# Optimization experiments

Hardware: AMD Instinct MI355X
Metric: run time of the kernel (lower is better)

The kernel has to match this reference:

```python
import jax, jax.numpy as jnp
import numpy as np


def setup_inputs() -> dict:
    key = jax.random.key(0)
    k1, k2 = jax.random.split(key)
    D, N, M = 256, 1024, 1024
    z_x = jax.random.normal(k1, (1, D, N), dtype=jnp.float32)
    z_y = jax.random.normal(k2, (1, D, M), dtype=jnp.float32)
    return {"z_x": z_x, "z_y": z_y}


def reference(z_x, z_y):
    # squeeze().t(): (1, d, N) -> (N, d)
    x = jnp.squeeze(z_x).T  # (N, d)
    y = jnp.squeeze(z_y).T  # (M, d)
    # L1 compare: s[i, j] = -sum_d |x[i, d] - y[j, d]|  -> (N, M)
    s = -jnp.sum(jnp.abs(x[:, None, :] - y[None, :, :]), axis=-1)
    a = jax.nn.softmax(s, axis=1)  # row-wise softmax
    b = jax.nn.softmax(s, axis=0)  # column-wise softmax
    a = a + b - a * b              # soft union of alignments
    return jnp.sum(a * s) / jnp.sum(a)
```

## Files before the change

### kernel.cpp

```cpp
#include <hip/hip_runtime.h>
#include <math.h>


#define DD 256
#define NN 1024
#define DS 4
#define CH (DD / DS)

__device__ __forceinline__ float waveMax(float v) {
  #pragma unroll
  for (int off = 32; off; off >>= 1) v = fmaxf(v, __shfl_xor(v, off, 64));
  return v;
}
__device__ __forceinline__ float waveSum(float v) {
  #pragma unroll
  for (int off = 32; off; off >>= 1) v += __shfl_xor(v, off, 64);
  return v;
}
__device__ __forceinline__ float blockMax(float v, float* red) {
  v = waveMax(v);
  __syncthreads();
  if ((threadIdx.x & 63) == 0) red[threadIdx.x >> 6] = v;
  __syncthreads();
  return fmaxf(fmaxf(red[0], red[1]), fmaxf(red[2], red[3]));
}
__device__ __forceinline__ float blockSum(float v, float* red) {
  v = waveSum(v);
  __syncthreads();
  if ((threadIdx.x & 63) == 0) red[threadIdx.x >> 6] = v;
  __syncthreads();
  return red[0] + red[1] + red[2] + red[3];
}


__global__ __launch_bounds__(256)
void scompute_kernel(const float* __restrict__ zx, const float* __restrict__ zy,
                     float* __restrict__ Sp, float* __restrict__ accum) {
  const int h  = blockIdx.z;
  const int i0 = blockIdx.y * 64;
  const int j0 = blockIdx.x * 128;
  const int t  = threadIdx.x;
  const int g  = t >> 5;
  const int c  = t & 31;
  if ((blockIdx.x | blockIdx.y | blockIdx.z) == 0 && t == 0) {
    accum[0] = 0.f; accum[1] = 0.f;
  }

  __shared__ float xs[CH * 64];
  {
    const float4* __restrict__ X4 = (const float4*)zx;
    float4* xs4 = (float4*)xs;
    #pragma unroll
    for (int k = t; k < CH * 16; k += 256)
      xs4[k] = X4[(h * CH + (k >> 4)) * (NN / 4) + (i0 >> 2) + (k & 15)];
  }
  __syncthreads();

  float acc[8][4];
  #pragma unroll
  for (int r = 0; r < 8; ++r)
    #pragma unroll
    for (int q = 0; q < 4; ++q) acc[r][q] = 0.f;

  const float4* __restrict__ yp =
      (const float4*)zy + (size_t)(h * CH) * (NN / 4) + (j0 >> 2) + c;
  #pragma unroll 4
  for (int d = 0; d < CH; ++d) {
    const float4 yv = yp[d * (NN / 4)];
    const float* xr = xs + d * 64 + g * 8;
    #pragma unroll
    for (int r = 0; r < 8; ++r) {
      const float xv = xr[r];
      acc[r][0] += fabsf(xv - yv.x);
      acc[r][1] += fabsf(xv - yv.y);
      acc[r][2] += fabsf(xv - yv.z);
      acc[r][3] += fabsf(xv - yv.w);
    }
  }

  float4* __restrict__ S4 = (float4*)Sp + (size_t)h * (NN * NN / 4);
  #pragma unroll
  for (int r = 0; r < 8; ++r)
    S4[(i0 + g * 8 + r) * (NN / 4) + (j0 >> 2) + c] =
        make_float4(acc[r][0], acc[r][1], acc[r][2], acc[r][3]);
}

__global__ __launch_bounds__(256)
void rowstats_kernel(float* __restrict__ Sp,
                     float* __restrict__ rmax, float* __restrict__ rsum) {
  __shared__ float red[4];
  const int t = threadIdx.x;
  const int row0 = blockIdx.x * 4;
  float4* S4 = (float4*)Sp;
  #pragma unroll
  for (int rr = 0; rr < 4; ++rr) {
    const int row = row0 + rr;
    float4 p = S4[row * (NN / 4) + t];
    #pragma unroll
    for (int hh = 1; hh < DS; ++hh) {
      const float4 q = S4[hh * (NN * NN / 4) + row * (NN / 4) + t];
      p.x += q.x; p.y += q.y; p.z += q.z; p.w += q.w;
    }
    S4[row * (NN / 4) + t] = p;
    float m = fmaxf(fmaxf(-p.x, -p.y), fmaxf(-p.z, -p.w));
    m = blockMax(m, red);
    float l = __expf(-p.x - m) + __expf(-p.y - m) +
              __expf(-p.z - m) + __expf(-p.w - m);
    l = blockSum(l, red);
    if (t == 0) { rmax[row] = m; rsum[row] = l; }
  }
}

__global__ __launch_bounds__(256)
void colstats_kernel(const float* __restrict__ Sp,
                     float* __restrict__ pm, float* __restrict__ ps) {
  const int t = threadIdx.x;
  const int r0 = blockIdx.x * 16;
  const float4* S4 = (const float4*)Sp;
  float4 m = make_float4(-1e30f, -1e30f, -1e30f, -1e30f);
  #pragma unroll 4
  for (int i = 0; i < 16; ++i) {
    const float4 p = S4[(r0 + i) * (NN / 4) + t];
    m.x = fmaxf(m.x, -p.x); m.y = fmaxf(m.y, -p.y);
    m.z = fmaxf(m.z, -p.z); m.w = fmaxf(m.w, -p.w);
  }
  float4 l = make_float4(0.f, 0.f, 0.f, 0.f);
  #pragma unroll 4
  for (int i = 0; i < 16; ++i) {
    const float4 p = S4[(r0 + i) * (NN / 4) + t];
    l.x += __expf(-p.x - m.x); l.y += __expf(-p.y - m.y);
    l.z += __expf(-p.z - m.z); l.w += __expf(-p.w - m.w);
  }
  ((float4*)pm)[blockIdx.x * (NN / 4) + t] = m;
  ((float4*)ps)[blockIdx.x * (NN / 4) + t] = l;
}

__global__ __launch_bounds__(256)
void colcombine_kernel(const float* __restrict__ pm, const float* __restrict__ ps,
                       float* __restrict__ cmax, float* __restrict__ csum) {
  const int j = blockIdx.x * 256 + threadIdx.x;
  float m = -1e30f;
  #pragma unroll 8
  for (int k = 0; k < 64; ++k) m = fmaxf(m, pm[k * NN + j]);
  float l = 0.f;
  #pragma unroll 8
  for (int k = 0; k < 64; ++k) l += __expf(pm[k * NN + j] - m) * ps[k * NN + j];
  cmax[j] = m; csum[j] = l;
}

__global__ __launch_bounds__(256)
void final_kernel(const float* __restrict__ Sp,
                  const float* __restrict__ rmax, const float* __restrict__ rsum,
                  const float* __restrict__ cmax, const float* __restrict__ csum,
                  float* __restrict__ accum) {
  __shared__ float redn[4], redd[4];
  const int t = threadIdx.x;
  const int row0 = blockIdx.x * 4;
  const float4* S4 = (const float4*)Sp;
  const float4 cm = ((const float4*)cmax)[t];
  const float4 cs = ((const float4*)csum)[t];
  float un = 0.f, ud = 0.f;
  #pragma unroll
  for (int rr = 0; rr < 4; ++rr) {
    const int row = row0 + rr;
    const float rm = rmax[row];
    const float ri = 1.f / rsum[row];
    const float4 p = S4[row * (NN / 4) + t];
    {
      const float s = -p.x;
      const float a = __expf(s - rm) * ri;
      const float b = __expf(s - cm.x) / cs.x;
      const float u = a + b - a * b;
      un += u * s; ud += u;
    }
    {
      const float s = -p.y;
      const float a = __expf(s - rm) * ri;
      const float b = __expf(s - cm.y) / cs.y;
      const float u = a + b - a * b;
      un += u * s; ud += u;
    }
    {
      const float s = -p.z;
      const float a = __expf(s - rm) * ri;
      const float b = __expf(s - cm.z) / cs.z;
      const float u = a + b - a * b;
      un += u * s; ud += u;
    }
    {
      const float s = -p.w;
      const float a = __expf(s - rm) * ri;
      const float b = __expf(s - cm.w) / cs.w;
      const float u = a + b - a * b;
      un += u * s; ud += u;
    }
  }
  un = waveSum(un); ud = waveSum(ud);
  if ((t & 63) == 0) { redn[t >> 6] = un; redd[t >> 6] = ud; }
  __syncthreads();
  if (t == 0) {
    atomicAdd(&accum[0], redn[0] + redn[1] + redn[2] + redn[3]);
    atomicAdd(&accum[1], redd[0] + redd[1] + redd[2] + redd[3]);
  }
}

__global__ void finalize_kernel(const float* __restrict__ accum, float* __restrict__ out) {
  out[0] = accum[0] / accum[1];
}


#define TJ  128
#define NCH (NN / TJ)
#define BLK 256

__global__ __launch_bounds__(BLK)
void stats2_kernel(const float* __restrict__ zx, const float* __restrict__ zy,
                   float* __restrict__ partM, float* __restrict__ partS) {
  const int side = blockIdx.z;
  const float* __restrict__ X = side ? zy : zx;
  const float* __restrict__ Y = side ? zx : zy;
  const int j0 = blockIdx.x * TJ;
  const int i0 = blockIdx.y * 8;
  const int t  = threadIdx.x;
  const int rg = t >> 5;
  const int c  = t & 31;

  __shared__ float xs[8 * DD];
  for (int k = t; k < 8 * DD; k += BLK)
    xs[k] = X[(k >> 3) * NN + i0 + (k & 7)];
  __syncthreads();

  const float4* __restrict__ Y4 = (const float4*)Y;
  const int yb = (j0 >> 2) + c;
  float4 acc = make_float4(0.f, 0.f, 0.f, 0.f);
  #pragma unroll 8
  for (int d = 0; d < DD; ++d) {
    const float4 yv = Y4[d * (NN / 4) + yb];
    const float xv = xs[d * 8 + rg];
    acc.x += fabsf(xv - yv.x);
    acc.y += fabsf(xv - yv.y);
    acc.z += fabsf(xv - yv.z);
    acc.w += fabsf(xv - yv.w);
  }

  float m = fmaxf(fmaxf(-acc.x, -acc.y), fmaxf(-acc.z, -acc.w));
  #pragma unroll
  for (int off = 16; off > 0; off >>= 1) m = fmaxf(m, __shfl_xor(m, off, 32));
  float p = __expf(-acc.x - m) + __expf(-acc.y - m) +
            __expf(-acc.z - m) + __expf(-acc.w - m);
  #pragma unroll
  for (int off = 16; off > 0; off >>= 1) p += __shfl_xor(p, off, 32);

  if (c == 0) {
    const int idx = side * (NCH * NN) + blockIdx.x * NN + (i0 + rg);
    partM[idx] = m;
    partS[idx] = p;
  }
}

__global__ __launch_bounds__(BLK)
void combine_kernel(const float* __restrict__ partM, const float* __restrict__ partS,
                    float* __restrict__ rmax, float* __restrict__ rsum,
                    float* __restrict__ cmax, float* __restrict__ csum,
                    float* __restrict__ accum) {
  const int gid = blockIdx.x * BLK + threadIdx.x;
  if (gid == 0) { accum[0] = 0.f; accum[1] = 0.f; }
  const int sd = gid >> 10;
  const int i  = gid & (NN - 1);
  float mk[NCH], sk[NCH];
  #pragma unroll
  for (int k = 0; k < NCH; ++k) {
    mk[k] = partM[sd * (NCH * NN) + k * NN + i];
    sk[k] = partS[sd * (NCH * NN) + k * NN + i];
  }
  float m = mk[0];
  #pragma unroll
  for (int k = 1; k < NCH; ++k) m = fmaxf(m, mk[k]);
  float s = 0.f;
  #pragma unroll
  for (int k = 0; k < NCH; ++k) s += __expf(mk[k] - m) * sk[k];
  if (sd == 0) { rmax[i] = m; rsum[i] = s; }
  else         { cmax[i] = m; csum[i] = s; }
}

__global__ __launch_bounds__(BLK)
void final2_kernel(const float* __restrict__ zx, const float* __restrict__ zy,
                   const float* __restrict__ rmax, const float* __restrict__ rsum,
                   const float* __restrict__ cmax, const float* __restrict__ csum,
                   float* __restrict__ accum) {
  const int j0 = blockIdx.x * TJ;
  const int i0 = blockIdx.y * 8;
  const int t  = threadIdx.x;
  const int rg = t >> 5;
  const int c  = t & 31;

  __shared__ float xs[8 * DD];
  __shared__ float redn[4], redd[4];
  for (int k = t; k < 8 * DD; k += BLK)
    xs[k] = zx[(k >> 3) * NN + i0 + (k & 7)];
  __syncthreads();

  const float4* __restrict__ Y4 = (const float4*)zy;
  const int yb = (j0 >> 2) + c;
  float4 acc = make_float4(0.f, 0.f, 0.f, 0.f);
  #pragma unroll 8
  for (int d = 0; d < DD; ++d) {
    const float4 yv = Y4[d * (NN / 4) + yb];
    const float xv = xs[d * 8 + rg];
    acc.x += fabsf(xv - yv.x);
    acc.y += fabsf(xv - yv.y);
    acc.z += fabsf(xv - yv.z);
    acc.w += fabsf(xv - yv.w);
  }

  const int i = i0 + rg;
  const float rm = rmax[i];
  const float ri = 1.f / rsum[i];
  const float4 cm = ((const float4*)cmax)[yb];
  const float4 cs = ((const float4*)csum)[yb];

  float un = 0.f, ud = 0.f;
  {
    const float s = -acc.x;
    const float a = __expf(s - rm) * ri;
    const float b = __expf(s - cm.x) / cs.x;
    const float u = a + b - a * b;
    un += u * s; ud += u;
  }
  {
    const float s = -acc.y;
    const float a = __expf(s - rm) * ri;
    const float b = __expf(s - cm.y) / cs.y;
    const float u = a + b - a * b;
    un += u * s; ud += u;
  }
  {
    const float s = -acc.z;
    const float a = __expf(s - rm) * ri;
    const float b = __expf(s - cm.z) / cs.z;
    const float u = a + b - a * b;
    un += u * s; ud += u;
  }
  {
    const float s = -acc.w;
    const float a = __expf(s - rm) * ri;
    const float b = __expf(s - cm.w) / cs.w;
    const float u = a + b - a * b;
    un += u * s; ud += u;
  }

  un = waveSum(un); ud = waveSum(ud);
  if ((t & 63) == 0) { redn[t >> 6] = un; redd[t >> 6] = ud; }
  __syncthreads();
  if (t == 0) {
    atomicAdd(&accum[0], redn[0] + redn[1] + redn[2] + redn[3]);
    atomicAdd(&accum[1], redd[0] + redd[1] + redd[2] + redd[3]);
  }
}


extern "C" void kernel_launch(void* const* d_in, const int* in_sizes, int n_in,
                              void* d_out, int out_size, void* d_ws, size_t ws_size,
                              hipStream_t stream) {
  const float* zx = (const float*)d_in[0];
  const float* zy = (const float*)d_in[1];
  float* ws  = (float*)d_ws;
  float* out = (float*)d_out;

  float* accum = ws;
  float* Sp    = ws + 16;
  float* pm    = Sp + DS * NN * NN;
  float* ps    = pm + 64 * NN;
  float* rmax  = ps + 64 * NN;
  float* rsum  = rmax + NN;
  float* cmax  = rsum + NN;
  float* csum  = cmax + NN;
  const size_t need = (size_t)((csum + NN) - ws) * sizeof(float);

  if (ws_size >= need) {
    dim3 g1(NN / 128, NN / 64, DS);
    scompute_kernel<<<g1, 256, 0, stream>>>(zx, zy, Sp, accum);
    rowstats_kernel<<<NN / 4, 256, 0, stream>>>(Sp, rmax, rsum);
    colstats_kernel<<<NN / 16, 256, 0, stream>>>(Sp, pm, ps);
    colcombine_kernel<<<NN / 256, 256, 0, stream>>>(pm, ps, cmax, csum);
    final_kernel<<<NN / 4, 256, 0, stream>>>(Sp, rmax, rsum, cmax, csum, accum);
    finalize_kernel<<<1, 1, 0, stream>>>(accum, out);
  } else {
    float* partM = ws + 16;
    float* partS = partM + 2 * NCH * NN;
    float* frmax = partS + 2 * NCH * NN;
    float* frsum = frmax + NN;
    float* fcmax = frsum + NN;
    float* fcsum = fcmax + NN;
    dim3 sgrid(NCH, NN / 8, 2);
    stats2_kernel<<<sgrid, BLK, 0, stream>>>(zx, zy, partM, partS);
    combine_kernel<<<(2 * NN) / BLK, BLK, 0, stream>>>(partM, partS,
                                                       frmax, frsum, fcmax, fcsum, accum);
    dim3 fgrid(NCH, NN / 8);
    final2_kernel<<<fgrid, BLK, 0, stream>>>(zx, zy, frmax, frsum, fcmax, fcsum, accum);
    finalize_kernel<<<1, 1, 0, stream>>>(accum, out);
  }
}
```

Measured before the change: 125.2 us.

## Fuse row/col stats, retile distance kernel, fold finalize into last block

Retiles the L1 distance kernel to 32x256 output tiles with vectorized shared-memory x loads, explicit y-register prefetch and launch bounds hinting two blocks per CU. It merges the row-stats and column-partial-stats passes into one kernel so the reduced S matrix is read once. Column partials grow to 256 per column, and the combine now splits them across four thread groups per column with a shared-memory merge. The separate finalize launch is replaced by a last-block-done atomic counter in the final kernel, adding a threadfence and counter atomics.

```diff
diff --git a/kernel.cpp b/kernel.cpp
--- a/kernel.cpp
+++ b/kernel.cpp
@@ -6,6 +6,7 @@
 #define NN 1024
 #define DS 4
 #define CH (DD / DS)
+#define NQ (NN / 4)
 
 __device__ __forceinline__ float waveMax(float v) {
   #pragma unroll
@@ -33,26 +34,53 @@
 }
 
 
-__global__ __launch_bounds__(256)
+#define SSTEP(YB, dd)                                                          \
+  {                                                                            \
+    const float* xp_ = xs + (dd) * 32 + g * 8;                                 \
+    const float4 xa = *(const float4*)xp_;                                     \
+    const float4 xb = *(const float4*)(xp_ + 4);                               \
+    acc[0][0] += fabsf(xa.x - YB.x); acc[0][1] += fabsf(xa.x - YB.y);          \
+    acc[0][2] += fabsf(xa.x - YB.z); acc[0][3] += fabsf(xa.x - YB.w);          \
+    acc[1][0] += fabsf(xa.y - YB.x); acc[1][1] += fabsf(xa.y - YB.y);          \
+    acc[1][2] += fabsf(xa.y - YB.z); acc[1][3] += fabsf(xa.y - YB.w);          \
+    acc[2][0] += fabsf(xa.z - YB.x); acc[2][1] += fabsf(xa.z - YB.y);          \
+    acc[2][2] += fabsf(xa.z - YB.z); acc[2][3] += fabsf(xa.z - YB.w);          \
+    acc[3][0] += fabsf(xa.w - YB.x); acc[3][1] += fabsf(xa.w - YB.y);          \
+    acc[3][2] += fabsf(xa.w - YB.z); acc[3][3] += fabsf(xa.w - YB.w);          \
+    acc[4][0] += fabsf(xb.x - YB.x); acc[4][1] += fabsf(xb.x - YB.y);          \
+    acc[4][2] += fabsf(xb.x - YB.z); acc[4][3] += fabsf(xb.x - YB.w);          \
+    acc[5][0] += fabsf(xb.y - YB.x); acc[5][1] += fabsf(xb.y - YB.y);          \
+    acc[5][2] += fabsf(xb.y - YB.z); acc[5][3] += fabsf(xb.y - YB.w);          \
+    acc[6][0] += fabsf(xb.z - YB.x); acc[6][1] += fabsf(xb.z - YB.y);          \
+    acc[6][2] += fabsf(xb.z - YB.z); acc[6][3] += fabsf(xb.z - YB.w);          \
+    acc[7][0] += fabsf(xb.w - YB.x); acc[7][1] += fabsf(xb.w - YB.y);          \
+    acc[7][2] += fabsf(xb.w - YB.z); acc[7][3] += fabsf(xb.w - YB.w);          \
+    const int dn_ = ((dd) + 4 < CH) ? (dd) + 4 : CH - 1;                       \
+    YB = yp[dn_ * NQ];                                                         \
+  }
+
+__global__ __launch_bounds__(256, 2)
 void scompute_kernel(const float* __restrict__ zx, const float* __restrict__ zy,
                      float* __restrict__ Sp, float* __restrict__ accum) {
   const int h  = blockIdx.z;
-  const int i0 = blockIdx.y * 64;
-  const int j0 = blockIdx.x * 128;
+  const int i0 = blockIdx.y * 32;
+  const int j0 = blockIdx.x * 256;
   const int t  = threadIdx.x;
-  const int g  = t >> 5;
-  const int c  = t & 31;
-  if ((blockIdx.x | blockIdx.y | blockIdx.z) == 0 && t == 0) {
-    accum[0] = 0.f; accum[1] = 0.f;
-  }
-
-  __shared__ float xs[CH * 64];
+  const int g  = t >> 6;
+  const int c  = t & 63;
+  if (t == 0 && (blockIdx.x | blockIdx.y | blockIdx.z) == 0) {
+    accum[0] = 0.f; accum[1] = 0.f; ((unsigned int*)accum)[2] = 0u;
+  }
+
+  __shared__ float xs[CH * 32];
   {
     const float4* __restrict__ X4 = (const float4*)zx;
     float4* xs4 = (float4*)xs;
     #pragma unroll
-    for (int k = t; k < CH * 16; k += 256)
-      xs4[k] = X4[(h * CH + (k >> 4)) * (NN / 4) + (i0 >> 2) + (k & 15)];
+    for (int k = t; k < CH * 8; k += 256) {
+      const int dd = k >> 3, rq = k & 7;
+      xs4[k] = X4[(h * CH + dd) * NQ + (i0 >> 2) + rq];
+    }
   }
   __syncthreads();
 
@@ -63,96 +91,102 @@
     for (int q = 0; q < 4; ++q) acc[r][q] = 0.f;
 
   const float4* __restrict__ yp =
-      (const float4*)zy + (size_t)(h * CH) * (NN / 4) + (j0 >> 2) + c;
-  #pragma unroll 4
-  for (int d = 0; d < CH; ++d) {
-    const float4 yv = yp[d * (NN / 4)];
-    const float* xr = xs + d * 64 + g * 8;
-    #pragma unroll
-    for (int r = 0; r < 8; ++r) {
-      const float xv = xr[r];
-      acc[r][0] += fabsf(xv - yv.x);
-      acc[r][1] += fabsf(xv - yv.y);
-      acc[r][2] += fabsf(xv - yv.z);
-      acc[r][3] += fabsf(xv - yv.w);
-    }
-  }
-
-  float4* __restrict__ S4 = (float4*)Sp + (size_t)h * (NN * NN / 4);
+      (const float4*)zy + (size_t)(h * CH) * NQ + (j0 >> 2) + c;
+  float4 y0 = yp[0 * NQ];
+  float4 y1 = yp[1 * NQ];
+  float4 y2 = yp[2 * NQ];
+  float4 y3 = yp[3 * NQ];
+
+  #pragma unroll 1
+  for (int d = 0; d < CH; d += 4) {
+    SSTEP(y0, d + 0)
+    SSTEP(y1, d + 1)
+    SSTEP(y2, d + 2)
+    SSTEP(y3, d + 3)
+  }
+
+  float4* __restrict__ S4 = (float4*)Sp + (size_t)h * (NN * NQ);
   #pragma unroll
   for (int r = 0; r < 8; ++r)
-    S4[(i0 + g * 8 + r) * (NN / 4) + (j0 >> 2) + c] =
+    S4[(i0 + g * 8 + r) * NQ + (j0 >> 2) + c] =
         make_float4(acc[r][0], acc[r][1], acc[r][2], acc[r][3]);
 }
 
 __global__ __launch_bounds__(256)
-void rowstats_kernel(float* __restrict__ Sp,
-                     float* __restrict__ rmax, float* __restrict__ rsum) {
+void rowcolstats_kernel(float* __restrict__ Sp,
+                        float* __restrict__ rmax, float* __restrict__ rsum,
+                        float* __restrict__ pm, float* __restrict__ ps) {
   __shared__ float red[4];
   const int t = threadIdx.x;
   const int row0 = blockIdx.x * 4;
   float4* S4 = (float4*)Sp;
-  #pragma unroll
-  for (int rr = 0; rr < 4; ++rr) {
-    const int row = row0 + rr;
-    float4 p = S4[row * (NN / 4) + t];
+  float4 p[4];
+  #pragma unroll
+  for (int r = 0; r < 4; ++r) {
+    float4 v = S4[(row0 + r) * NQ + t];
     #pragma unroll
     for (int hh = 1; hh < DS; ++hh) {
-      const float4 q = S4[hh * (NN * NN / 4) + row * (NN / 4) + t];
-      p.x += q.x; p.y += q.y; p.z += q.z; p.w += q.w;
-    }
-    S4[row * (NN / 4) + t] = p;
-    float m = fmaxf(fmaxf(-p.x, -p.y), fmaxf(-p.z, -p.w));
+      const float4 q = S4[(size_t)hh * (NN * NQ) + (row0 + r) * NQ + t];
+      v.x += q.x; v.y += q.y; v.z += q.z; v.w += q.w;
+    }
+    S4[(row0 + r) * NQ + t] = v;
+    p[r] = v;
+  }
+  #pragma unroll
+  for (int r = 0; r < 4; ++r) {
+    float m = fmaxf(fmaxf(-p[r].x, -p[r].y), fmaxf(-p[r].z, -p[r].w));
     m = blockMax(m, red);
-    float l = __expf(-p.x - m) + __expf(-p.y - m) +
-              __expf(-p.z - m) + __expf(-p.w - m);
+    float l = __expf(-p[r].x - m) + __expf(-p[r].y - m) +
+              __expf(-p[r].z - m) + __expf(-p[r].w - m);
     l = blockSum(l, red);
-    if (t == 0) { rmax[row] = m; rsum[row] = l; }
-  }
-}
-
-__global__ __launch_bounds__(256)
-void colstats_kernel(const float* __restrict__ Sp,
-                     float* __restrict__ pm, float* __restrict__ ps) {
-  const int t = threadIdx.x;
-  const int r0 = blockIdx.x * 16;
-  const float4* S4 = (const float4*)Sp;
-  float4 m = make_float4(-1e30f, -1e30f, -1e30f, -1e30f);
-  #pragma unroll 4
-  for (int i = 0; i < 16; ++i) {
-    const float4 p = S4[(r0 + i) * (NN / 4) + t];
-    m.x = fmaxf(m.x, -p.x); m.y = fmaxf(m.y, -p.y);
-    m.z = fmaxf(m.z, -p.z); m.w = fmaxf(m.w, -p.w);
-  }
-  float4 l = make_float4(0.f, 0.f, 0.f, 0.f);
-  #pragma unroll 4
-  for (int i = 0; i < 16; ++i) {
-    const float4 p = S4[(r0 + i) * (NN / 4) + t];
-    l.x += __expf(-p.x - m.x); l.y += __expf(-p.y - m.y);
-    l.z += __expf(-p.z - m.z); l.w += __expf(-p.w - m.w);
-  }
-  ((float4*)pm)[blockIdx.x * (NN / 4) + t] = m;
-  ((float4*)ps)[blockIdx.x * (NN / 4) + t] = l;
+    if (t == 0) { rmax[row0 + r] = m; rsum[row0 + r] = l; }
+  }
+  float4 cm = make_float4(-1e30f, -1e30f, -1e30f, -1e30f);
+  #pragma unroll
+  for (int r = 0; r < 4; ++r) {
+    cm.x = fmaxf(cm.x, -p[r].x); cm.y = fmaxf(cm.y, -p[r].y);
+    cm.z = fmaxf(cm.z, -p[r].z); cm.w = fmaxf(cm.w, -p[r].w);
+  }
+  float4 cl = make_float4(0.f, 0.f, 0.f, 0.f);
+  #pragma unroll
+  for (int r = 0; r < 4; ++r) {
+    cl.x += __expf(-p[r].x - cm.x); cl.y += __expf(-p[r].y - cm.y);
+    cl.z += __expf(-p[r].z - cm.z); cl.w += __expf(-p[r].w - cm.w);
+  }
+  ((float4*)pm)[blockIdx.x * NQ + t] = cm;
+  ((float4*)ps)[blockIdx.x * NQ + t] = cl;
 }
 
 __global__ __launch_bounds__(256)
 void colcombine_kernel(const float* __restrict__ pm, const float* __restrict__ ps,
                        float* __restrict__ cmax, float* __restrict__ csum) {
-  const int j = blockIdx.x * 256 + threadIdx.x;
+  __shared__ float sm[4][64], sl[4][64];
+  const int t  = threadIdx.x;
+  const int jl = t & 63;
+  const int pc = t >> 6;
+  const int j  = blockIdx.x * 64 + jl;
   float m = -1e30f;
   #pragma unroll 8
-  for (int k = 0; k < 64; ++k) m = fmaxf(m, pm[k * NN + j]);
+  for (int k = 0; k < 64; ++k) m = fmaxf(m, pm[(pc * 64 + k) * NN + j]);
   float l = 0.f;
   #pragma unroll 8
-  for (int k = 0; k < 64; ++k) l += __expf(pm[k * NN + j] - m) * ps[k * NN + j];
-  cmax[j] = m; csum[j] = l;
+  for (int k = 0; k < 64; ++k)
+    l += __expf(pm[(pc * 64 + k) * NN + j] - m) * ps[(pc * 64 + k) * NN + j];
+  sm[pc][jl] = m; sl[pc][jl] = l;
+  __syncthreads();
+  if (pc == 0) {
+    float M = fmaxf(fmaxf(sm[0][jl], sm[1][jl]), fmaxf(sm[2][jl], sm[3][jl]));
+    float L = sl[0][jl] * __expf(sm[0][jl] - M) + sl[1][jl] * __expf(sm[1][jl] - M) +
+              sl[2][jl] * __expf(sm[2][jl] - M) + sl[3][jl] * __expf(sm[3][jl] - M);
+    cmax[j] = M; csum[j] = L;
+  }
 }
 
 __global__ __launch_bounds__(256)
 void final_kernel(const float* __restrict__ Sp,
                   const float* __restrict__ rmax, const float* __restrict__ rsum,
                   const float* __restrict__ cmax, const float* __restrict__ csum,
-                  float* __restrict__ accum) {
+                  float* __restrict__ accum, float* __restrict__ out) {
   __shared__ float redn[4], redd[4];
   const int t = threadIdx.x;
   const int row0 = blockIdx.x * 4;
@@ -161,11 +195,11 @@
   const float4 cs = ((const float4*)csum)[t];
   float un = 0.f, ud = 0.f;
   #pragma unroll
-  for (int rr = 0; rr < 4; ++rr) {
-    const int row = row0 + rr;
+  for (int r = 0; r < 4; ++r) {
+    const int row = row0 + r;
     const float rm = rmax[row];
     const float ri = 1.f / rsum[row];
-    const float4 p = S4[row * (NN / 4) + t];
+    const float4 p = S4[row * NQ + t];
     {
       const float s = -p.x;
       const float a = __expf(s - rm) * ri;
@@ -201,11 +235,15 @@
   if (t == 0) {
     atomicAdd(&accum[0], redn[0] + redn[1] + redn[2] + redn[3]);
     atomicAdd(&accum[1], redd[0] + redd[1] + redd[2] + redd[3]);
-  }
-}
-
-__global__ void finalize_kernel(const float* __restrict__ accum, float* __restrict__ out) {
-  out[0] = accum[0] / accum[1];
+    __threadfence();
+    unsigned int* cnt = (unsigned int*)accum + 2;
+    const unsigned int old = atomicAdd(cnt, 1u);
+    if (old == gridDim.x - 1) {
+      const float n = atomicAdd(&accum[0], 0.f);
+      const float d = atomicAdd(&accum[1], 0.f);
+      out[0] = n / d;
+    }
+  }
 }
 
 
@@ -235,7 +273,7 @@
   float4 acc = make_float4(0.f, 0.f, 0.f, 0.f);
   #pragma unroll 8
   for (int d = 0; d < DD; ++d) {
-    const float4 yv = Y4[d * (NN / 4) + yb];
+    const float4 yv = Y4[d * NQ + yb];
     const float xv = xs[d * 8 + rg];
     acc.x += fabsf(xv - yv.x);
     acc.y += fabsf(xv - yv.y);
@@ -305,7 +343,7 @@
   float4 acc = make_float4(0.f, 0.f, 0.f, 0.f);
   #pragma unroll 8
   for (int d = 0; d < DD; ++d) {
-    const float4 yv = Y4[d * (NN / 4) + yb];
+    const float4 yv = Y4[d * NQ + yb];
     const float xv = xs[d * 8 + rg];
     acc.x += fabsf(xv - yv.x);
     acc.y += fabsf(xv - yv.y);
@@ -358,6 +396,10 @@
   }
 }
 
+__global__ void finalize_kernel(const float* __restrict__ accum, float* __restrict__ out) {
+  out[0] = accum[0] / accum[1];
+}
+
 
 extern "C" void kernel_launch(void* const* d_in, const int* in_sizes, int n_in,
                               void* d_out, int out_size, void* d_ws, size_t ws_size,
@@ -370,21 +412,19 @@
   float* accum = ws;
   float* Sp    = ws + 16;
   float* pm    = Sp + DS * NN * NN;
-  float* ps    = pm + 64 * NN;
-  float* rmax  = ps + 64 * NN;
+  float* ps    = pm + 256 * NN;
+  float* rmax  = ps + 256 * NN;
   float* rsum  = rmax + NN;
   float* cmax  = rsum + NN;
   float* csum  = cmax + NN;
   const size_t need = (size_t)((csum + NN) - ws) * sizeof(float);
 
   if (ws_size >= need) {
-    dim3 g1(NN / 128, NN / 64, DS);
+    dim3 g1(NN / 256, NN / 32, DS);
     scompute_kernel<<<g1, 256, 0, stream>>>(zx, zy, Sp, accum);
-    rowstats_kernel<<<NN / 4, 256, 0, stream>>>(Sp, rmax, rsum);
-    colstats_kernel<<<NN / 16, 256, 0, stream>>>(Sp, pm, ps);
-    colcombine_kernel<<<NN / 256, 256, 0, stream>>>(pm, ps, cmax, csum);
-    final_kernel<<<NN / 4, 256, 0, stream>>>(Sp, rmax, rsum, cmax, csum, accum);
-    finalize_kernel<<<1, 1, 0, stream>>>(accum, out);
+    rowcolstats_kernel<<<NN / 4, 256, 0, stream>>>(Sp, rmax, rsum, pm, ps);
+    colcombine_kernel<<<NN / 64, 256, 0, stream>>>(pm, ps, cmax, csum);
+    final_kernel<<<NN / 4, 256, 0, stream>>>(Sp, rmax, rsum, cmax, csum, accum, out);
   } else {
     float* partM = ws + 16;
     float* partS = partM + 2 * NCH * NN;
```

After: 124.5 us. No clear change (-0.6%).
